# Kernel optimization log

Measured on AMD Instinct MI355X. Metric: run time of the kernel, lower is better.

The kernel has to match this reference:

```python
import jax, jax.numpy as jnp
import numpy as np

B, N, C, H, DEPTH, MLP = 8, 1024, 768, 12, 8, 3072
HD = C // H
SCALE = HD ** -0.5
EPS = 1e-5


def layer_norm(x, g, b):
    mu = jnp.mean(x, -1, keepdims=True)
    var = jnp.mean((x - mu) ** 2, -1, keepdims=True)
    return (x - mu) / jnp.sqrt(var + EPS) * g + b


def setup_inputs() -> dict:
    key = jax.random.key(0)
    ks = jax.random.split(key, 8)
    s = 0.02
    return {
        "x": jax.random.normal(ks[0], (B, N, C), jnp.float32),
        "ln1_g": jnp.ones((DEPTH, C), jnp.float32),
        "ln1_b": jnp.zeros((DEPTH, C), jnp.float32),
        "wqkv": jax.random.normal(ks[1], (DEPTH, C, 3 * C), jnp.float32) * s,
        "wproj": jax.random.normal(ks[2], (DEPTH, C, C), jnp.float32) * s,
        "bproj": jnp.zeros((DEPTH, C), jnp.float32),
        "ln2_g": jnp.ones((DEPTH, C), jnp.float32),
        "ln2_b": jnp.zeros((DEPTH, C), jnp.float32),
        "w1": jax.random.normal(ks[3], (DEPTH, C, MLP), jnp.float32) * s,
        "b1": jnp.zeros((DEPTH, MLP), jnp.float32),
        "w2": jax.random.normal(ks[4], (DEPTH, MLP, C), jnp.float32) * s,
        "b2": jnp.zeros((DEPTH, C), jnp.float32),
    }


def reference(x, ln1_g, ln1_b, wqkv, wproj, bproj, ln2_g, ln2_b, w1, b1, w2, b2):
    def body(h, p):
        g1, be1, wq, wp, bp, g2, be2, wf1, bf1, wf2, bf2 = p
        # --- attention block: Residual(PreNorm(SelfAttention)) ---
        y = layer_norm(h, g1, be1)
        qkv = (y @ wq).reshape(B, N, 3, H, HD)
        qkv = jnp.transpose(qkv, (2, 0, 3, 1, 4))  # [3, B, H, N, HD]
        q, k, v = qkv[0], qkv[1], qkv[2]
        logits = jnp.einsum("bhnd,bhmd->bhnm", q, k) * SCALE
        # source applies softmax twice (faithful to original)
        attn = jax.nn.softmax(jax.nn.softmax(logits, axis=-1), axis=-1)
        o = jnp.einsum("bhnm,bhmd->bhnd", attn, v)
        o = jnp.transpose(o, (0, 2, 1, 3)).reshape(B, N, C)
        h = h + o @ wp + bp
        # --- FFN block: Residual(PreNorm(FeedForward)) ---
        y2 = layer_norm(h, g2, be2)
        f = jax.nn.relu(y2 @ wf1 + bf1) @ wf2 + bf2
        return h + f, None

    out, _ = jax.lax.scan(body, x, (ln1_g, ln1_b, wqkv, wproj, bproj, ln2_g, ln2_b, w1, b1, w2, b2))
    return out
```

## Files before the change

### kernel.cpp

```cpp
#include <hip/hip_runtime.h>
#include <hip/hip_bf16.h>

#define DEPTHL 8
#define BZ 8
#define SEQ 1024
#define CDIM 768
#define HEADS 12
#define HDIM 64
#define MLPD 3072
#define TOK (BZ*SEQ)
#define QKVN (3*CDIM)

typedef __attribute__((ext_vector_type(8))) short vshort8;
typedef __attribute__((ext_vector_type(4))) short vshort4;
typedef __attribute__((ext_vector_type(4))) float vfloat4;

__device__ __forceinline__ short bf16_bits(float f) {
  union { float f; unsigned u; } x; x.f = f;
  unsigned r = (x.u + 0x7FFFu + ((x.u >> 16) & 1u)) >> 16;
  return (short)r;
}

__device__ __forceinline__ unsigned pk_bf16(float a, float b) {
  unsigned r;
  asm("v_cvt_pk_bf16_f32 %0, %1, %2" : "=v"(r) : "v"(a), "v"(b));
  return r;
}

#define GL16(g, l) __builtin_amdgcn_global_load_lds( \
    (const __attribute__((address_space(1))) unsigned int*)(g), \
    (__attribute__((address_space(3))) unsigned int*)(l), 16, 0, 0)

__global__ __launch_bounds__(256) void wconv_t(const float* __restrict__ in,
                                               short* __restrict__ out,
                                               int K, int N) {
  __shared__ float tile[32][33];
  const long d = blockIdx.z;
  in  += d * (long)K * N;
  out += d * (long)N * K;
  const int n0 = blockIdx.x * 32, k0 = blockIdx.y * 32;
  const int tx = threadIdx.x & 31, ty = threadIdx.x >> 5;
#pragma unroll
  for (int i = 0; i < 4; i++)
    tile[ty + 8*i][tx] = in[(long)(k0 + ty + 8*i) * N + n0 + tx];
  __syncthreads();
#pragma unroll
  for (int i = 0; i < 4; i++)
    out[(long)(n0 + ty + 8*i) * K + k0 + tx] = bf16_bits(tile[tx][ty + 8*i]);
}

__global__ __launch_bounds__(256) void vtrans(const short* __restrict__ qkv,
                                              short* __restrict__ vt) {
  __shared__ short tile[32][34];
  const int bh = blockIdx.z;
  const int b = bh / HEADS, hh = bh % HEADS;
  const int t0 = blockIdx.x * 32, d0 = blockIdx.y * 32;
  const int tx = threadIdx.x & 31, ty = threadIdx.x >> 5;
  const short* src = qkv + ((long)b * SEQ + t0) * QKVN + 2 * CDIM + hh * HDIM + d0;
#pragma unroll
  for (int i = 0; i < 4; i++)
    tile[ty + 8*i][tx] = src[(long)(ty + 8*i) * QKVN + tx];
  __syncthreads();
  short* dst = vt + (long)bh * HDIM * SEQ + (long)d0 * SEQ + t0;
#pragma unroll
  for (int i = 0; i < 4; i++)
    dst[(long)(ty + 8*i) * SEQ + tx] = tile[tx][ty + 8*i];
}

__global__ __launch_bounds__(192) void ln_fwd(const float* __restrict__ h,
                                              const float* __restrict__ g,
                                              const float* __restrict__ be,
                                              short* __restrict__ y) {
  __shared__ float red[3];
  const int row = blockIdx.x;
  const int tid = threadIdx.x;
  const float4 v = ((const float4*)(h + (long)row * CDIM))[tid];
  float s = v.x + v.y + v.z + v.w;
#pragma unroll
  for (int m = 32; m >= 1; m >>= 1) s += __shfl_xor(s, m);
  if ((tid & 63) == 0) red[tid >> 6] = s;
  __syncthreads();
  const float mu = (red[0] + red[1] + red[2]) * (1.0f / CDIM);
  float dx = v.x - mu, dy = v.y - mu, dz = v.z - mu, dw = v.w - mu;
  float q = dx*dx + dy*dy + dz*dz + dw*dw;
  __syncthreads();
#pragma unroll
  for (int m = 32; m >= 1; m >>= 1) q += __shfl_xor(q, m);
  if ((tid & 63) == 0) red[tid >> 6] = q;
  __syncthreads();
  const float rstd = rsqrtf((red[0] + red[1] + red[2]) * (1.0f / CDIM) + 1e-5f);
  const float4 g4 = ((const float4*)g)[tid];
  const float4 b4 = ((const float4*)be)[tid];
  vshort4 o;
  o[0] = bf16_bits(dx * rstd * g4.x + b4.x);
  o[1] = bf16_bits(dy * rstd * g4.y + b4.y);
  o[2] = bf16_bits(dz * rstd * g4.z + b4.z);
  o[3] = bf16_bits(dw * rstd * g4.w + b4.w);
  *(vshort4*)(y + (long)row * CDIM + tid * 4) = o;
}

template<int EPI>
__global__ __launch_bounds__(256) void gemm_bt(const short* __restrict__ A,
                                               const short* __restrict__ Bt,
                                               const float* __restrict__ bias,
                                               void* __restrict__ Cout,
                                               int M, int N, int K) {
  __shared__ short As[128 * 64];
  __shared__ short Bs[128 * 64];
  const int tid = threadIdx.x;
  const int wid = tid >> 6, lane = tid & 63;
  const int lg = lane >> 4, lr = lane & 15;
  const int wm = wid >> 1, wn = wid & 1;

  const int gx = gridDim.x;
  const int nwg = gx * gridDim.y;
  int flat = blockIdx.y * gx + blockIdx.x;
  flat = (flat & 7) * (nwg >> 3) + (flat >> 3);
  const long bx = flat % gx;
  const long by = flat / gx;

  vfloat4 acc[4][4];
#pragma unroll
  for (int i = 0; i < 4; i++)
#pragma unroll
    for (int j = 0; j < 4; j++) acc[i][j] = (vfloat4){0.f, 0.f, 0.f, 0.f};

  const short* Abase = A  + by * 128 * (long)K;
  const short* Bbase = Bt + bx * 128 * (long)K;

  for (int kk = 0; kk < K; kk += 64) {
    __syncthreads();
#pragma unroll
    for (int ch = 0; ch < 4; ch++) {
      const int dst = tid * 16 + ch * 4096;
      const int off = dst ^ (((dst >> 7) & 7) << 4);
      const long srow = off >> 7;
      const int scol = (off & 127) >> 1;
      GL16(Abase + srow * K + kk + scol, As + (dst >> 1));
      GL16(Bbase + srow * K + kk + scol, Bs + (dst >> 1));
    }
    __syncthreads();
#pragma unroll
    for (int kh = 0; kh < 2; kh++) {
      vshort8 a[4], b[4];
#pragma unroll
      for (int mt = 0; mt < 4; mt++) {
        const int row = wm * 64 + mt * 16 + lr;
        int byt = row * 128 + kh * 64 + lg * 16;
        byt ^= (row & 7) << 4;
        a[mt] = *(const vshort8*)((const char*)As + byt);
      }
#pragma unroll
      for (int nt = 0; nt < 4; nt++) {
        const int row = wn * 64 + nt * 16 + lr;
        int byt = row * 128 + kh * 64 + lg * 16;
        byt ^= (row & 7) << 4;
        b[nt] = *(const vshort8*)((const char*)Bs + byt);
      }
#pragma unroll
      for (int mt = 0; mt < 4; mt++)
#pragma unroll
        for (int nt = 0; nt < 4; nt++)
          acc[mt][nt] = __builtin_amdgcn_mfma_f32_16x16x32_bf16(a[mt], b[nt], acc[mt][nt], 0, 0, 0);
    }
  }

  const long row0 = by * 128 + wm * 64;
  const long col0 = bx * 128 + wn * 64;
#pragma unroll
  for (int mt = 0; mt < 4; mt++) {
#pragma unroll
    for (int nt = 0; nt < 4; nt++) {
      const long col = col0 + nt * 16 + lr;
      float bv = 0.f;
      if (EPI != 0) bv = bias[col];
#pragma unroll
      for (int r = 0; r < 4; r++) {
        const long row = row0 + mt * 16 + lg * 4 + r;
        float v = acc[mt][nt][r];
        if (EPI == 0) {
          ((short*)Cout)[row * N + col] = bf16_bits(v);
        } else if (EPI == 1) {
          v += bv; v = v > 0.f ? v : 0.f;
          ((short*)Cout)[row * N + col] = bf16_bits(v);
        } else {
          float* hp = (float*)Cout + row * N + col;
          *hp = *hp + v + bv;
        }
      }
    }
  }
}

__global__ __launch_bounds__(256, 4) void attn_fused4(const short* __restrict__ qkv,
                                                      const short* __restrict__ vt,
                                                      short* __restrict__ o) {
  __shared__ __align__(16) short P_lds[4 * 4096];
  __shared__ float redm[4][16], redz[4][16], redt[4][16];
  int flat = blockIdx.y * 64 + blockIdx.x;
  flat = (flat & 7) * (6144 >> 3) + (flat >> 3);
  const int qt = flat & 63;
  const int bh = flat >> 6;
  const int b = bh / HEADS, hh = bh % HEADS;
  const int tid = threadIdx.x, wid = tid >> 6, lane = tid & 63;
  const int lg = lane >> 4, lr = lane & 15;
  const long tokbase = (long)b * SEQ;
  const short* qbase = qkv + tokbase * QKVN + hh * HDIM;
  const short* kbase = qkv + tokbase * QKVN + CDIM + hh * HDIM;
  const short* vtb = vt + (long)bh * HDIM * SEQ;
  char* Pw = (char*)P_lds + wid * 8192;

  vshort8 qf[2];
#pragma unroll
  for (int ks = 0; ks < 2; ks++)
    qf[ks] = *(const vshort8*)(qbase + (long)(qt * 16 + lr) * QKVN + ks * 32 + lg * 8);

  vfloat4 s[16];
#pragma unroll
  for (int bb = 0; bb < 4; bb++) {
    vshort8 kf[8];
#pragma unroll
    for (int u = 0; u < 4; u++) {
      const int n0 = wid * 256 + (bb * 4 + u) * 16;
#pragma unroll
      for (int ks = 0; ks < 2; ks++)
        kf[u * 2 + ks] = *(const vshort8*)(kbase + (long)(n0 + lr) * QKVN + ks * 32 + lg * 8);
    }
#pragma unroll
    for (int u = 0; u < 4; u++) {
      vfloat4 acc = (vfloat4){0.f, 0.f, 0.f, 0.f};
      acc = __builtin_amdgcn_mfma_f32_16x16x32_bf16(kf[u * 2 + 0], qf[0], acc, 0, 0, 0);
      acc = __builtin_amdgcn_mfma_f32_16x16x32_bf16(kf[u * 2 + 1], qf[1], acc, 0, 0, 0);
      s[bb * 4 + u] = acc;
    }
  }

  float mt16[16];
#pragma unroll
  for (int i = 0; i < 16; i++)
    mt16[i] = fmaxf(fmaxf(s[i][0], s[i][1]), fmaxf(s[i][2], s[i][3]));
#pragma unroll
  for (int st = 8; st >= 1; st >>= 1)
#pragma unroll
    for (int i = 0; i < 8; i++) if (i < st) mt16[i] = fmaxf(mt16[i], mt16[i + st]);
  float m = mt16[0];
  m = fmaxf(m, __shfl_xor(m, 16));
  m = fmaxf(m, __shfl_xor(m, 32));
  if (lane < 16) redm[wid][lr] = m;
  __syncthreads();
  m = fmaxf(fmaxf(redm[0][lr], redm[1][lr]), fmaxf(redm[2][lr], redm[3][lr]));
  const float msc = m * 0.125f;

  float zt[16];
#pragma unroll
  for (int i = 0; i < 16; i++) {
    float e0 = __expf(fmaf(s[i][0], 0.125f, -msc));
    float e1 = __expf(fmaf(s[i][1], 0.125f, -msc));
    float e2 = __expf(fmaf(s[i][2], 0.125f, -msc));
    float e3 = __expf(fmaf(s[i][3], 0.125f, -msc));
    s[i][0] = e0; s[i][1] = e1; s[i][2] = e2; s[i][3] = e3;
    zt[i] = (e0 + e1) + (e2 + e3);
  }
#pragma unroll
  for (int st = 8; st >= 1; st >>= 1)
#pragma unroll
    for (int i = 0; i < 8; i++) if (i < st) zt[i] += zt[i + st];
  float z = zt[0];
  z += __shfl_xor(z, 16);
  z += __shfl_xor(z, 32);
  if (lane < 16) redz[wid][lr] = z;
  __syncthreads();
  z = (redz[0][lr] + redz[1][lr]) + (redz[2][lr] + redz[3][lr]);
  const float rz = 1.0f / z;

  float tt[16];
#pragma unroll
  for (int i = 0; i < 16; i++) {
    float p0 = __expf(s[i][0] * rz);
    float p1 = __expf(s[i][1] * rz);
    float p2 = __expf(s[i][2] * rz);
    float p3 = __expf(s[i][3] * rz);
    s[i][0] = p0; s[i][1] = p1; s[i][2] = p2; s[i][3] = p3;
    tt[i] = (p0 + p1) + (p2 + p3);
  }
#pragma unroll
  for (int st = 8; st >= 1; st >>= 1)
#pragma unroll
    for (int i = 0; i < 8; i++) if (i < st) tt[i] += tt[i + st];
  float t2 = tt[0];
  t2 += __shfl_xor(t2, 16);
  t2 += __shfl_xor(t2, 32);
  if (lane < 16) redt[wid][lr] = t2;
  __syncthreads();
  t2 = (redt[0][lr] + redt[1][lr]) + (redt[2][lr] + redt[3][lr]);
  const float rt = 1.0f / t2;

#pragma unroll
  for (int i = 0; i < 16; i++) {
    const int byt = (lr * 512 + i * 32 + lg * 8) ^ ((lr & 7) << 4);
    uint2 pk;
    pk.x = pk_bf16(s[i][0] * rt, s[i][1] * rt);
    pk.y = pk_bf16(s[i][2] * rt, s[i][3] * rt);
    *(uint2*)(Pw + byt) = pk;
  }

  vfloat4 oacc[4];
#pragma unroll
  for (int dt = 0; dt < 4; dt++) oacc[dt] = (vfloat4){0.f, 0.f, 0.f, 0.f};
#pragma unroll
  for (int j = 0; j < 8; j++) {
    const int abyt = (lr * 512 + j * 64 + lg * 16) ^ ((lr & 7) << 4);
    vshort8 af = *(const vshort8*)(Pw + abyt);
#pragma unroll
    for (int dt = 0; dt < 4; dt++) {
      vshort8 vb = *(const vshort8*)(vtb + (long)(dt * 16 + lr) * SEQ + wid * 256 + j * 32 + lg * 8);
      oacc[dt] = __builtin_amdgcn_mfma_f32_16x16x32_bf16(af, vb, oacc[dt], 0, 0, 0);
    }
  }

#pragma unroll
  for (int dt = 0; dt < 4; dt++)
#pragma unroll
    for (int r = 0; r < 4; r++)
      *(float*)(Pw + ((lg * 4 + r) * 64 + dt * 16 + lr) * 4) = oacc[dt][r];
  __syncthreads();

  const int q = tid >> 4, d0 = (tid & 15) * 4;
  float4 a0 = *(const float4*)((const char*)P_lds + 0 * 8192 + (q * 64 + d0) * 4);
  float4 a1 = *(const float4*)((const char*)P_lds + 1 * 8192 + (q * 64 + d0) * 4);
  float4 a2 = *(const float4*)((const char*)P_lds + 2 * 8192 + (q * 64 + d0) * 4);
  float4 a3 = *(const float4*)((const char*)P_lds + 3 * 8192 + (q * 64 + d0) * 4);
  float ox = (a0.x + a1.x) + (a2.x + a3.x);
  float oy = (a0.y + a1.y) + (a2.y + a3.y);
  float oz = (a0.z + a1.z) + (a2.z + a3.z);
  float ow = (a0.w + a1.w) + (a2.w + a3.w);
  uint2 ob;
  ob.x = pk_bf16(ox, oy);
  ob.y = pk_bf16(oz, ow);
  *(uint2*)(o + (tokbase + qt * 16 + q) * CDIM + hh * HDIM + d0) = ob;
}

extern "C" void kernel_launch(void* const* d_in, const int* in_sizes, int n_in,
                              void* d_out, int out_size, void* d_ws, size_t ws_size,
                              hipStream_t stream) {
  const float* x     = (const float*)d_in[0];
  const float* ln1_g = (const float*)d_in[1];
  const float* ln1_b = (const float*)d_in[2];
  const float* wqkv  = (const float*)d_in[3];
  const float* wproj = (const float*)d_in[4];
  const float* bproj = (const float*)d_in[5];
  const float* ln2_g = (const float*)d_in[6];
  const float* ln2_b = (const float*)d_in[7];
  const float* w1    = (const float*)d_in[8];
  const float* b1    = (const float*)d_in[9];
  const float* w2    = (const float*)d_in[10];
  const float* b2    = (const float*)d_in[11];
  float* h = (float*)d_out;

  char* ws = (char*)d_ws;
  short* wqkv_t  = (short*)ws; ws += (size_t)DEPTHL * QKVN * CDIM * 2;
  short* wproj_t = (short*)ws; ws += (size_t)DEPTHL * CDIM * CDIM * 2;
  short* w1_t    = (short*)ws; ws += (size_t)DEPTHL * MLPD * CDIM * 2;
  short* w2_t    = (short*)ws; ws += (size_t)DEPTHL * CDIM * MLPD * 2;
  short* ybf     = (short*)ws; ws += (size_t)TOK * CDIM * 2;
  short* qkvbf   = (short*)ws; ws += (size_t)TOK * QKVN * 2;
  short* obf     = (short*)ws; ws += (size_t)TOK * CDIM * 2;
  short* f1bf    = (short*)ws; ws += (size_t)TOK * MLPD * 2;
  short* vtb     = f1bf;

  hipMemcpyAsync(h, x, (size_t)TOK * CDIM * sizeof(float), hipMemcpyDeviceToDevice, stream);

  wconv_t<<<dim3(QKVN / 32, CDIM / 32, DEPTHL), 256, 0, stream>>>(wqkv, wqkv_t, CDIM, QKVN);
  wconv_t<<<dim3(CDIM / 32, CDIM / 32, DEPTHL), 256, 0, stream>>>(wproj, wproj_t, CDIM, CDIM);
  wconv_t<<<dim3(MLPD / 32, CDIM / 32, DEPTHL), 256, 0, stream>>>(w1, w1_t, CDIM, MLPD);
  wconv_t<<<dim3(CDIM / 32, MLPD / 32, DEPTHL), 256, 0, stream>>>(w2, w2_t, MLPD, CDIM);

  for (int l = 0; l < DEPTHL; l++) {
    ln_fwd<<<TOK, 192, 0, stream>>>(h, ln1_g + l * CDIM, ln1_b + l * CDIM, ybf);
    gemm_bt<0><<<dim3(QKVN / 128, TOK / 128), 256, 0, stream>>>(
        ybf, wqkv_t + (size_t)l * QKVN * CDIM, nullptr, qkvbf, TOK, QKVN, CDIM);
    vtrans<<<dim3(SEQ / 32, HDIM / 32, BZ * HEADS), 256, 0, stream>>>(qkvbf, vtb);
    attn_fused4<<<dim3(SEQ / 16, BZ * HEADS), 256, 0, stream>>>(qkvbf, vtb, obf);
    gemm_bt<2><<<dim3(CDIM / 128, TOK / 128), 256, 0, stream>>>(
        obf, wproj_t + (size_t)l * CDIM * CDIM, bproj + l * CDIM, h, TOK, CDIM, CDIM);
    ln_fwd<<<TOK, 192, 0, stream>>>(h, ln2_g + l * CDIM, ln2_b + l * CDIM, ybf);
    gemm_bt<1><<<dim3(MLPD / 128, TOK / 128), 256, 0, stream>>>(
        ybf, w1_t + (size_t)l * MLPD * CDIM, b1 + l * MLPD, f1bf, TOK, MLPD, CDIM);
    gemm_bt<2><<<dim3(CDIM / 128, TOK / 128), 256, 0, stream>>>(
        f1bf, w2_t + (size_t)l * CDIM * MLPD, b2 + l * CDIM, h, TOK, CDIM, MLPD);
  }
}
```

Before: 3.314 ms.

## Triple-buffer GEMM K-loop with async prefetch; one-wave-per-row LayerNorm

The GEMM main loop moves from a single 64-wide K tile with two barriers per step to a three-stage ring of 32-wide K tiles. Loads run two stages ahead, guarded by vmcnt waits, with one barrier per iteration and raised wave priority around the MFMA block. This is meant to hide global-to-LDS load latency behind matrix math, at the cost of smaller K steps and more loop iterations. LayerNorm is also rewritten so each 64-lane wave handles a whole row, four rows per block, which removes the shared-memory reductions and block barriers.

```diff
diff --git a/kernel.cpp b/kernel.cpp
--- a/kernel.cpp
+++ b/kernel.cpp
@@ -67,36 +67,46 @@
     dst[(long)(ty + 8*i) * SEQ + tx] = tile[tx][ty + 8*i];
 }
 
-__global__ __launch_bounds__(192) void ln_fwd(const float* __restrict__ h,
+__global__ __launch_bounds__(256) void ln_fwd(const float* __restrict__ h,
                                               const float* __restrict__ g,
                                               const float* __restrict__ be,
                                               short* __restrict__ y) {
-  __shared__ float red[3];
-  const int row = blockIdx.x;
-  const int tid = threadIdx.x;
-  const float4 v = ((const float4*)(h + (long)row * CDIM))[tid];
-  float s = v.x + v.y + v.z + v.w;
+  const int row = blockIdx.x * 4 + (threadIdx.x >> 6);
+  const int lane = threadIdx.x & 63;
+  const float4* hr = (const float4*)(h + (long)row * CDIM);
+  const float4 v0 = hr[lane], v1 = hr[lane + 64], v2 = hr[lane + 128];
+  float s = (v0.x + v0.y + v0.z + v0.w) + (v1.x + v1.y + v1.z + v1.w)
+          + (v2.x + v2.y + v2.z + v2.w);
 #pragma unroll
   for (int m = 32; m >= 1; m >>= 1) s += __shfl_xor(s, m);
-  if ((tid & 63) == 0) red[tid >> 6] = s;
-  __syncthreads();
-  const float mu = (red[0] + red[1] + red[2]) * (1.0f / CDIM);
-  float dx = v.x - mu, dy = v.y - mu, dz = v.z - mu, dw = v.w - mu;
-  float q = dx*dx + dy*dy + dz*dz + dw*dw;
-  __syncthreads();
+  const float mu = s * (1.0f / CDIM);
+  float d0x = v0.x - mu, d0y = v0.y - mu, d0z = v0.z - mu, d0w = v0.w - mu;
+  float d1x = v1.x - mu, d1y = v1.y - mu, d1z = v1.z - mu, d1w = v1.w - mu;
+  float d2x = v2.x - mu, d2y = v2.y - mu, d2z = v2.z - mu, d2w = v2.w - mu;
+  float q = (d0x*d0x + d0y*d0y + d0z*d0z + d0w*d0w)
+          + (d1x*d1x + d1y*d1y + d1z*d1z + d1w*d1w)
+          + (d2x*d2x + d2y*d2y + d2z*d2z + d2w*d2w);
 #pragma unroll
   for (int m = 32; m >= 1; m >>= 1) q += __shfl_xor(q, m);
-  if ((tid & 63) == 0) red[tid >> 6] = q;
-  __syncthreads();
-  const float rstd = rsqrtf((red[0] + red[1] + red[2]) * (1.0f / CDIM) + 1e-5f);
-  const float4 g4 = ((const float4*)g)[tid];
-  const float4 b4 = ((const float4*)be)[tid];
-  vshort4 o;
-  o[0] = bf16_bits(dx * rstd * g4.x + b4.x);
-  o[1] = bf16_bits(dy * rstd * g4.y + b4.y);
-  o[2] = bf16_bits(dz * rstd * g4.z + b4.z);
-  o[3] = bf16_bits(dw * rstd * g4.w + b4.w);
-  *(vshort4*)(y + (long)row * CDIM + tid * 4) = o;
+  const float rstd = rsqrtf(q * (1.0f / CDIM) + 1e-5f);
+  const float4* gp = (const float4*)g;
+  const float4* bp = (const float4*)be;
+  short* yr = y + (long)row * CDIM;
+#pragma unroll
+  for (int c = 0; c < 3; c++) {
+    const float4 g4 = gp[lane + c * 64];
+    const float4 b4 = bp[lane + c * 64];
+    float dx = (c == 0 ? d0x : c == 1 ? d1x : d2x);
+    float dy = (c == 0 ? d0y : c == 1 ? d1y : d2y);
+    float dz = (c == 0 ? d0z : c == 1 ? d1z : d2z);
+    float dw = (c == 0 ? d0w : c == 1 ? d1w : d2w);
+    vshort4 o;
+    o[0] = bf16_bits(dx * rstd * g4.x + b4.x);
+    o[1] = bf16_bits(dy * rstd * g4.y + b4.y);
+    o[2] = bf16_bits(dz * rstd * g4.z + b4.z);
+    o[3] = bf16_bits(dw * rstd * g4.w + b4.w);
+    *(vshort4*)(yr + c * 256 + lane * 4) = o;
+  }
 }
 
 template<int EPI>
@@ -105,8 +115,8 @@
                                                const float* __restrict__ bias,
                                                void* __restrict__ Cout,
                                                int M, int N, int K) {
-  __shared__ short As[128 * 64];
-  __shared__ short Bs[128 * 64];
+  __shared__ short As[3 * 128 * 32];
+  __shared__ short Bs[3 * 128 * 32];
   const int tid = threadIdx.x;
   const int wid = tid >> 6, lane = tid & 63;
   const int lg = lane >> 4, lr = lane & 15;
@@ -119,50 +129,66 @@
   const long bx = flat % gx;
   const long by = flat / gx;
 
-  vfloat4 acc[4][4];
-#pragma unroll
-  for (int i = 0; i < 4; i++)
-#pragma unroll
-    for (int j = 0; j < 4; j++) acc[i][j] = (vfloat4){0.f, 0.f, 0.f, 0.f};
-
+  const int NT = K >> 5;
   const short* Abase = A  + by * 128 * (long)K;
   const short* Bbase = Bt + bx * 128 * (long)K;
 
-  for (int kk = 0; kk < K; kk += 64) {
-    __syncthreads();
-#pragma unroll
-    for (int ch = 0; ch < 4; ch++) {
+  vfloat4 acc[4][4];
+#pragma unroll
+  for (int i = 0; i < 4; i++)
+#pragma unroll
+    for (int j = 0; j < 4; j++) acc[i][j] = (vfloat4){0.f, 0.f, 0.f, 0.f};
+
+  auto STAGE = [&](int T) {
+    const int bo = (T % 3) * (128 * 32);
+#pragma unroll
+    for (int ch = 0; ch < 2; ch++) {
       const int dst = tid * 16 + ch * 4096;
-      const int off = dst ^ (((dst >> 7) & 7) << 4);
-      const long srow = off >> 7;
-      const int scol = (off & 127) >> 1;
-      GL16(Abase + srow * K + kk + scol, As + (dst >> 1));
-      GL16(Bbase + srow * K + kk + scol, Bs + (dst >> 1));
-    }
-    __syncthreads();
-#pragma unroll
-    for (int kh = 0; kh < 2; kh++) {
-      vshort8 a[4], b[4];
-#pragma unroll
-      for (int mt = 0; mt < 4; mt++) {
-        const int row = wm * 64 + mt * 16 + lr;
-        int byt = row * 128 + kh * 64 + lg * 16;
-        byt ^= (row & 7) << 4;
-        a[mt] = *(const vshort8*)((const char*)As + byt);
-      }
-#pragma unroll
-      for (int nt = 0; nt < 4; nt++) {
-        const int row = wn * 64 + nt * 16 + lr;
-        int byt = row * 128 + kh * 64 + lg * 16;
-        byt ^= (row & 7) << 4;
-        b[nt] = *(const vshort8*)((const char*)Bs + byt);
-      }
-#pragma unroll
-      for (int mt = 0; mt < 4; mt++)
-#pragma unroll
-        for (int nt = 0; nt < 4; nt++)
-          acc[mt][nt] = __builtin_amdgcn_mfma_f32_16x16x32_bf16(a[mt], b[nt], acc[mt][nt], 0, 0, 0);
-    }
+      const int off = dst ^ (((dst >> 6) & 3) << 4);
+      const long srow = off >> 6;
+      const int scol = (off & 63) >> 1;
+      GL16(Abase + srow * K + T * 32 + scol, As + bo + (dst >> 1));
+      GL16(Bbase + srow * K + T * 32 + scol, Bs + bo + (dst >> 1));
+    }
+  };
+
+  STAGE(0);
+  STAGE(1);
+  asm volatile("s_waitcnt vmcnt(4)" ::: "memory");
+  __builtin_amdgcn_sched_barrier(0);
+  __builtin_amdgcn_s_barrier();
+
+  for (int T = 0; T < NT; ++T) {
+    if (T + 2 < NT) STAGE(T + 2);
+    const short* Ab = As + (T % 3) * (128 * 32);
+    const short* Bb = Bs + (T % 3) * (128 * 32);
+    vshort8 a[4], b[4];
+#pragma unroll
+    for (int mt = 0; mt < 4; mt++) {
+      int byt = (wm * 64 + mt * 16 + lr) * 64 + lg * 16;
+      byt ^= ((byt >> 6) & 3) << 4;
+      a[mt] = *(const vshort8*)((const char*)Ab + byt);
+    }
+#pragma unroll
+    for (int nt = 0; nt < 4; nt++) {
+      int byt = (wn * 64 + nt * 16 + lr) * 64 + lg * 16;
+      byt ^= ((byt >> 6) & 3) << 4;
+      b[nt] = *(const vshort8*)((const char*)Bb + byt);
+    }
+    __builtin_amdgcn_s_setprio(1);
+#pragma unroll
+    for (int mt = 0; mt < 4; mt++)
+#pragma unroll
+      for (int nt = 0; nt < 4; nt++)
+        acc[mt][nt] = __builtin_amdgcn_mfma_f32_16x16x32_bf16(a[mt], b[nt], acc[mt][nt], 0, 0, 0);
+    __builtin_amdgcn_s_setprio(0);
+    if (T + 2 < NT) {
+      asm volatile("s_waitcnt vmcnt(4)" ::: "memory");
+    } else {
+      asm volatile("s_waitcnt vmcnt(0)" ::: "memory");
+    }
+    __builtin_amdgcn_sched_barrier(0);
+    __builtin_amdgcn_s_barrier();
   }
 
   const long row0 = by * 128 + wm * 64;
@@ -376,14 +402,14 @@
   wconv_t<<<dim3(CDIM / 32, MLPD / 32, DEPTHL), 256, 0, stream>>>(w2, w2_t, MLPD, CDIM);
 
   for (int l = 0; l < DEPTHL; l++) {
-    ln_fwd<<<TOK, 192, 0, stream>>>(h, ln1_g + l * CDIM, ln1_b + l * CDIM, ybf);
+    ln_fwd<<<TOK / 4, 256, 0, stream>>>(h, ln1_g + l * CDIM, ln1_b + l * CDIM, ybf);
     gemm_bt<0><<<dim3(QKVN / 128, TOK / 128), 256, 0, stream>>>(
         ybf, wqkv_t + (size_t)l * QKVN * CDIM, nullptr, qkvbf, TOK, QKVN, CDIM);
     vtrans<<<dim3(SEQ / 32, HDIM / 32, BZ * HEADS), 256, 0, stream>>>(qkvbf, vtb);
     attn_fused4<<<dim3(SEQ / 16, BZ * HEADS), 256, 0, stream>>>(qkvbf, vtb, obf);
     gemm_bt<2><<<dim3(CDIM / 128, TOK / 128), 256, 0, stream>>>(
         obf, wproj_t + (size_t)l * CDIM * CDIM, bproj + l * CDIM, h, TOK, CDIM, CDIM);
-    ln_fwd<<<TOK, 192, 0, stream>>>(h, ln2_g + l * CDIM, ln2_b + l * CDIM, ybf);
+    ln_fwd<<<TOK / 4, 256, 0, stream>>>(h, ln2_g + l * CDIM, ln2_b + l * CDIM, ybf);
     gemm_bt<1><<<dim3(MLPD / 128, TOK / 128), 256, 0, stream>>>(
         ybf, w1_t + (size_t)l * MLPD * CDIM, b1 + l * MLPD, f1bf, TOK, MLPD, CDIM);
     gemm_bt<2><<<dim3(CDIM / 128, TOK / 128), 256, 0, stream>>>(
```

After: 3.468 ms. +4.6%, slower.
